# Optimization experiments

Measured on AMD Instinct MI355X. Metric: run time of the kernel, lower is better.

Reference implementation:

```python
import jax, jax.numpy as jnp
import numpy as np

G, N, F_IN, H, C = 128, 512, 128, 128, 10
LAMB = 1.0
NEG_SLOPE = 0.2
P_EDGE = 32.0 / N  # avg degree ~32


def setup_inputs() -> dict:
    key = jax.random.key(0)
    ks = jax.random.split(key, 12)
    x = jax.random.normal(ks[0], (G, N, F_IN), dtype=jnp.float32)
    # symmetric 0/1 adjacency without self loops (per-graph dense block)
    a = (jax.random.uniform(ks[1], (G, N, N)) < P_EDGE).astype(jnp.float32)
    adj = jnp.maximum(a, jnp.swapaxes(a, 1, 2)) * (1.0 - jnp.eye(N, dtype=jnp.float32))

    def lin(k, fi, fo):
        return (jax.random.normal(k, (fi, fo), dtype=jnp.float32) / np.float32(np.sqrt(fi)))

    return {
        "x": x, "adj": adj,
        "W1": lin(ks[2], F_IN, H), "b1": jnp.zeros((H,), jnp.float32),
        "W2": lin(ks[3], H, H), "b2": jnp.zeros((H,), jnp.float32),
        "W3": lin(ks[4], H, H), "b3": jnp.zeros((H,), jnp.float32),
        "att1_s": 0.1 * jax.random.normal(ks[5], (H,), dtype=jnp.float32),
        "att1_d": 0.1 * jax.random.normal(ks[6], (H,), dtype=jnp.float32),
        "att2_s": 0.1 * jax.random.normal(ks[7], (H,), dtype=jnp.float32),
        "att2_d": 0.1 * jax.random.normal(ks[8], (H,), dtype=jnp.float32),
        "Wl1": lin(ks[9], 2 * H, H), "bl1": jnp.zeros((H,), jnp.float32),
        "Wl2": lin(ks[10], H, H // 2), "bl2": jnp.zeros((H // 2,), jnp.float32),
        "Wl3": lin(ks[11], H // 2, C), "bl3": jnp.zeros((C,), jnp.float32),
    }


def gcn(x, adj, W, b):
    # GCNConv: D^{-1/2} (A + I) D^{-1/2} X W + b  (self-loop weight 1, edge weights in adj)
    deg = adj.sum(-1) + 1.0                              # [G, n]
    dinv = jax.lax.rsqrt(deg)
    xw = x @ W                                           # [G, n, H]
    agg = jnp.einsum('gij,gjf->gif', adj, dinv[..., None] * xw)
    return dinv[..., None] * agg + (dinv * dinv)[..., None] * xw + b


def info_score(x, adj):
    # HGP-SL node information score: row-wise L1 norm of (I - D^{-1} A) X
    deg = jnp.maximum(adj.sum(-1), 1.0)
    agg = jnp.einsum('gij,gjf->gif', adj, x) / deg[..., None]
    return jnp.sum(jnp.abs(x - agg), axis=-1)            # [G, n]


def hgpsl_pool(x, adj, att_s, att_d, k):
    # top-k node selection by information score, then structure learning:
    # dense (sample=False) path: e_ij = leaky_relu(att.[x_i||x_j]) + lamb*A_ij, softmax over j
    s = info_score(x, adj)
    _, idx = jax.lax.top_k(s, k)                         # [G, k]
    xk = jnp.take_along_axis(x, idx[..., None], axis=1)  # [G, k, H]
    g = jnp.arange(x.shape[0])[:, None, None]
    ak = adj[g, idx[:, :, None], idx[:, None, :]]        # induced adjacency [G, k, k]
    e = jax.nn.leaky_relu((xk @ att_s)[:, :, None] + (xk @ att_d)[:, None, :], NEG_SLOPE)
    attn = jax.nn.softmax(e + LAMB * ak, axis=-1)        # new learned edge weights
    return xk, attn


def readout(x):
    # gmp || gap over nodes
    return jnp.concatenate([x.max(axis=1), x.mean(axis=1)], axis=-1)


def reference(x, adj, W1, b1, W2, b2, W3, b3, att1_s, att1_d, att2_s, att2_d,
              Wl1, bl1, Wl2, bl2, Wl3, bl3):
    h = jax.nn.relu(gcn(x, adj, W1, b1))
    h, a1 = hgpsl_pool(h, adj, att1_s, att1_d, N // 2)
    x1 = readout(h)
    h = jax.nn.relu(gcn(h, a1, W2, b2))
    h, a2 = hgpsl_pool(h, a1, att2_s, att2_d, N // 4)
    x2 = readout(h)
    h = jax.nn.relu(gcn(h, a2, W3, b3))
    x3 = readout(h)
    z = jax.nn.relu(x1) + jax.nn.relu(x2) + jax.nn.relu(x3)
    z = jax.nn.relu(z @ Wl1 + bl1)
    z = jax.nn.relu(z @ Wl2 + bl2)
    return jax.nn.softmax(z @ Wl3 + bl3, axis=-1)
```

## Files before the change

kernel.cpp:

```cpp
#include <hip/hip_runtime.h>

#define Gg   128
#define N1   512
#define FH   128
#define K1   256
#define K2   128

typedef __bf16 bf16x8 __attribute__((ext_vector_type(8)));
typedef float  floatx4 __attribute__((ext_vector_type(4)));

__device__ inline float wredsum(float v) {
#pragma unroll
    for (int o = 32; o; o >>= 1) v += __shfl_xor(v, o, 64);
    return v;
}
__device__ inline float wredmax(float v) {
#pragma unroll
    for (int o = 32; o; o >>= 1) v = fmaxf(v, __shfl_xor(v, o, 64));
    return v;
}
__device__ inline unsigned short bf_rne(float x) {
    unsigned u = __float_as_uint(x);
    return (unsigned short)((u + 0x7fffu + ((u >> 16) & 1u)) >> 16);
}

__global__ __launch_bounds__(256) void k_prep(const float* __restrict__ adj,
        float* __restrict__ dinv_gcn, float* __restrict__ dinv_info) {
    int wave = threadIdx.x >> 6, lane = threadIdx.x & 63;
    long long row = (long long)blockIdx.x * 4 + wave;
    const float* ar = adj + row * N1;
    float s = 0.f;
#pragma unroll
    for (int c = 0; c < 2; ++c) {
        float4 v = *(const float4*)(ar + lane * 8 + c * 4);
        s += (v.x + v.y) + (v.z + v.w);
    }
    s = wredsum(s);
    if (lane == 0) {
        dinv_gcn[row]  = rsqrtf(s + 1.0f);
        dinv_info[row] = 1.0f / fmaxf(s, 1.0f);
    }
}

__global__ __launch_bounds__(256) void k_tsplit(const float* __restrict__ feat,
        unsigned short* __restrict__ Thi, unsigned short* __restrict__ Tmid,
        unsigned short* __restrict__ Tlo) {
    __shared__ float tile[64 * 65];
    int b = blockIdx.x;
    int g = b >> 4, rb = (b >> 1) & 7, cb = b & 1;
    int t = threadIdx.x;
    {
        int r0 = t >> 4, c4 = t & 15;
#pragma unroll
        for (int i = 0; i < 4; ++i) {
            int r = r0 + i * 16;
            float4 v = *(const float4*)(feat + ((long long)g * 512 + rb * 64 + r) * 128 + cb * 64 + c4 * 4);
            tile[r * 65 + c4 * 4 + 0] = v.x;
            tile[r * 65 + c4 * 4 + 1] = v.y;
            tile[r * 65 + c4 * 4 + 2] = v.z;
            tile[r * 65 + c4 * 4 + 3] = v.w;
        }
    }
    __syncthreads();
    int tf = t >> 2, chunk = t & 3;
    unsigned short hbuf[16] __attribute__((aligned(16)));
    unsigned short mbuf[16] __attribute__((aligned(16)));
    unsigned short lbuf[16] __attribute__((aligned(16)));
#pragma unroll
    for (int i = 0; i < 16; ++i) {
        int m = chunk * 16 + i;
        float v = tile[m * 65 + tf];
        unsigned short h = bf_rne(v);
        float fh = __uint_as_float((unsigned)h << 16);
        float r1 = v - fh;
        unsigned short md = bf_rne(r1);
        float fm = __uint_as_float((unsigned)md << 16);
        float r2 = r1 - fm;
        unsigned short lo = bf_rne(r2);
        hbuf[i] = h; mbuf[i] = md; lbuf[i] = lo;
    }
    long long obase = ((long long)g * 128 + cb * 64 + tf) * 512 + rb * 64 + chunk * 16;
    *(uint4*)(Thi + obase)      = *(const uint4*)&hbuf[0];
    *(uint4*)(Thi + obase + 8)  = *(const uint4*)&hbuf[8];
    *(uint4*)(Tmid + obase)     = *(const uint4*)&mbuf[0];
    *(uint4*)(Tmid + obase + 8) = *(const uint4*)&mbuf[8];
    *(uint4*)(Tlo + obase)      = *(const uint4*)&lbuf[0];
    *(uint4*)(Tlo + obase + 8)  = *(const uint4*)&lbuf[8];
}

template<int EPI>
__global__ __launch_bounds__(256) void k_aggmm(const float* __restrict__ adjf,
        const unsigned short* __restrict__ Bhi, const unsigned short* __restrict__ Bmid,
        const unsigned short* __restrict__ Blo,
        const float* __restrict__ dvec, const float* __restrict__ hx,
        const float* __restrict__ bias, float* __restrict__ outH, float* __restrict__ outS) {
    __shared__ unsigned short Al[128 * 40];
    __shared__ unsigned short Bls[3][128 * 40];
    __shared__ float sred[2][128];
    int b = blockIdx.x;
    int g  = (b & 7) + ((b >> 5) << 3);
    int rb = (b >> 3) & 3;
    int tid = threadIdx.x;
    int w = tid >> 6, lane = tid & 63;
    int wm = w >> 1, wn = w & 1;
    int ln = lane & 15, quad = lane >> 4;
    floatx4 acc[4][4];
#pragma unroll
    for (int i = 0; i < 4; ++i)
#pragma unroll
        for (int j = 0; j < 4; ++j) { floatx4 z = {0.f, 0.f, 0.f, 0.f}; acc[i][j] = z; }

    const long long arow0 = ((long long)g * 512 + rb * 128) * 512;
    for (int kk = 0; kk < 512; kk += 32) {
        __syncthreads();
#pragma unroll
        for (int i = 0; i < 4; ++i) {
            int id = tid + i * 256;
            int r = id >> 3, c = id & 7;
            float4 v = *(const float4*)(adjf + arow0 + (long long)r * 512 + kk + c * 4);
            ushort4 u;
            u.x = (unsigned short)(__float_as_uint(v.x) >> 16);
            u.y = (unsigned short)(__float_as_uint(v.y) >> 16);
            u.z = (unsigned short)(__float_as_uint(v.z) >> 16);
            u.w = (unsigned short)(__float_as_uint(v.w) >> 16);
            *(ushort4*)&Al[r * 40 + c * 4] = u;
        }
#pragma unroll
        for (int mB = 0; mB < 3; ++mB) {
            const unsigned short* Bp = (mB == 0) ? Bhi : (mB == 1 ? Bmid : Blo);
#pragma unroll
            for (int i = 0; i < 2; ++i) {
                int id = tid + i * 256;
                int r = id >> 2, c = id & 3;
                uint4 u = *(const uint4*)(Bp + ((long long)g * 128 + r) * 512 + kk + c * 8);
                *(uint4*)&Bls[mB][r * 40 + c * 8] = u;
            }
        }
        __syncthreads();
        bf16x8 af[4];
#pragma unroll
        for (int tm = 0; tm < 4; ++tm)
            af[tm] = *(const bf16x8*)&Al[(wm * 64 + tm * 16 + ln) * 40 + quad * 8];
#pragma unroll
        for (int s = 0; s < 3; ++s) {
#pragma unroll
            for (int tn = 0; tn < 4; ++tn) {
                bf16x8 bfr = *(const bf16x8*)&Bls[s][(wn * 64 + tn * 16 + ln) * 40 + quad * 8];
#pragma unroll
                for (int tm = 0; tm < 4; ++tm)
                    acc[tm][tn] = __builtin_amdgcn_mfma_f32_16x16x32_bf16(af[tm], bfr, acc[tm][tn], 0, 0, 0);
            }
        }
    }
    long long rowbase = (long long)g * 512 + rb * 128;
    if (EPI == 0) {
#pragma unroll
        for (int tm = 0; tm < 4; ++tm)
#pragma unroll
        for (int r = 0; r < 4; ++r) {
            int ml = wm * 64 + tm * 16 + quad * 4 + r;
            long long grow = rowbase + ml;
            float di = dvec[grow];
#pragma unroll
            for (int tn = 0; tn < 4; ++tn) {
                int nc = wn * 64 + tn * 16 + ln;
                float hv = hx[grow * 128 + nc];
                float o = fmaxf(fmaf(di, acc[tm][tn][r] + hv, bias[nc]), 0.f);
                outH[grow * 128 + nc] = o;
            }
        }
    } else {
#pragma unroll
        for (int tm = 0; tm < 4; ++tm)
#pragma unroll
        for (int r = 0; r < 4; ++r) {
            int ml = wm * 64 + tm * 16 + quad * 4 + r;
            long long grow = rowbase + ml;
            float di = dvec[grow];
            float v = 0.f;
#pragma unroll
            for (int tn = 0; tn < 4; ++tn) {
                int nc = wn * 64 + tn * 16 + ln;
                float hv = hx[grow * 128 + nc];
                v += fabsf(hv - acc[tm][tn][r] * di);
            }
            v += __shfl_xor(v, 1); v += __shfl_xor(v, 2);
            v += __shfl_xor(v, 4); v += __shfl_xor(v, 8);
            if (ln == 0) sred[wn][ml] = v;
        }
        __syncthreads();
        if (tid < 128) outS[rowbase + tid] = sred[0][tid] + sred[1][tid];
    }
}

__global__ __launch_bounds__(256) void k_gemm_rw(const float* __restrict__ A,
        const float* __restrict__ W, float* __restrict__ C,
        const float* __restrict__ rs) {
    __shared__ float Al[64][68];
    __shared__ float Wl[64][132];
    long long row0 = (long long)blockIdx.x * 64;
    int tid = threadIdx.x, tr = tid >> 4, tc = tid & 15;
    float acc[4][8] = {};
    for (int ch = 0; ch < 2; ++ch) {
        for (int p = tid; p < 1024; p += 256) {
            int r = p >> 4, c4 = p & 15;
            *(float4*)&Al[r][c4 * 4] = *(const float4*)(A + (row0 + r) * 128 + ch * 64 + c4 * 4);
        }
        for (int p = tid; p < 2048; p += 256) {
            int r = p >> 5, c4 = p & 31;
            *(float4*)&Wl[r][c4 * 4] = *(const float4*)(W + (ch * 64 + r) * 128 + c4 * 4);
        }
        __syncthreads();
        for (int k = 0; k < 64; ++k) {
            float4 w0 = *(const float4*)&Wl[k][tc * 8];
            float4 w1 = *(const float4*)&Wl[k][tc * 8 + 4];
            float w[8] = {w0.x, w0.y, w0.z, w0.w, w1.x, w1.y, w1.z, w1.w};
#pragma unroll
            for (int i = 0; i < 4; ++i) {
                float a = Al[tr * 4 + i][k];
#pragma unroll
                for (int j = 0; j < 8; ++j) acc[i][j] = fmaf(a, w[j], acc[i][j]);
            }
        }
        __syncthreads();
    }
#pragma unroll
    for (int i = 0; i < 4; ++i) {
        long long r = row0 + tr * 4 + i;
        float sc = rs ? rs[r] : 1.0f;
        *(float4*)(C + r * 128 + tc * 8)     = make_float4(sc * acc[i][0], sc * acc[i][1], sc * acc[i][2], sc * acc[i][3]);
        *(float4*)(C + r * 128 + tc * 8 + 4) = make_float4(sc * acc[i][4], sc * acc[i][5], sc * acc[i][6], sc * acc[i][7]);
    }
}

template<int NT, int KSEL>
__global__ __launch_bounds__(256) void k_topk(const float* __restrict__ s, int* __restrict__ idx) {
    __shared__ unsigned long long keys[NT];
    int g = blockIdx.x;
    const float* sg = s + g * NT;
    for (int t = threadIdx.x; t < NT; t += 256) {
        unsigned int b = __float_as_uint(sg[t]);
        unsigned int ord = (b & 0x80000000u) ? ~b : (b | 0x80000000u);
        keys[t] = ((unsigned long long)(~ord) << 32) | (unsigned int)t;
    }
    __syncthreads();
    for (int k = 2; k <= NT; k <<= 1) {
        for (int j = k >> 1; j > 0; j >>= 1) {
            for (int i = threadIdx.x; i < NT; i += 256) {
                int l = i ^ j;
                if (l > i) {
                    bool dir = ((i & k) == 0);
                    unsigned long long a = keys[i], b2 = keys[l];
                    bool sw = dir ? (a > b2) : (a < b2);
                    if (sw) { keys[i] = b2; keys[l] = a; }
                }
            }
            __syncthreads();
        }
    }
    for (int t = threadIdx.x; t < KSEL; t += 256)
        idx[g * KSEL + t] = (int)(keys[t] & 0xffffffffu);
}

template<int KK>
__global__ __launch_bounds__(256) void k_gather(const float* __restrict__ h, int srcN,
        const int* __restrict__ idx, const float* __restrict__ atts, const float* __restrict__ attd,
        float* __restrict__ xk, float* __restrict__ as_, float* __restrict__ ad_) {
    int wave = threadIdx.x >> 6, lane = threadIdx.x & 63;
    int r = blockIdx.x * 4 + wave;
    int g = r / KK;
    int j = idx[r];
    float2 v = *(const float2*)(h + ((long long)g * srcN + j) * 128 + lane * 2);
    *(float2*)(xk + (long long)r * 128 + lane * 2) = v;
    float2 sv = *(const float2*)(atts + lane * 2);
    float2 dv = *(const float2*)(attd + lane * 2);
    float ps = v.x * sv.x + v.y * sv.y;
    float pd = v.x * dv.x + v.y * dv.y;
    ps = wredsum(ps); pd = wredsum(pd);
    if (lane == 0) { as_[r] = ps; ad_[r] = pd; }
}

template<int KK, int SRCN>
__global__ __launch_bounds__(256) void k_attn(const float* __restrict__ adjSrc,
        const int* __restrict__ idx, const float* __restrict__ as_, const float* __restrict__ ad_,
        float* __restrict__ attn, float* __restrict__ dgo, float* __restrict__ dio) {
    constexpr int E = KK / 64;
    __shared__ int   idxL[KK];
    __shared__ float adL[KK];
    __shared__ float rowL[4][SRCN];
    int bpg = KK / 4;
    int g = blockIdx.x / bpg;
    int wave = threadIdx.x >> 6, lane = threadIdx.x & 63;
    int i = (blockIdx.x % bpg) * 4 + wave;
    for (int t = threadIdx.x; t < KK; t += 256) { idxL[t] = idx[g * KK + t]; adL[t] = ad_[g * KK + t]; }
    __syncthreads();
    int ri = idxL[i];
    const float* arow = adjSrc + ((long long)g * SRCN + ri) * SRCN;
    for (int c = lane; c < SRCN; c += 64) rowL[wave][c] = arow[c];
    float asi = as_[g * KK + i];
    float vals[E];
    float m = -1e30f;
#pragma unroll
    for (int e = 0; e < E; ++e) {
        int j = e * 64 + lane;
        float x = asi + adL[j];
        x = (x >= 0.f) ? x : 0.2f * x;
        x += rowL[wave][idxL[j]];
        vals[e] = x; m = fmaxf(m, x);
    }
    m = wredmax(m);
    float S = 0.f;
#pragma unroll
    for (int e = 0; e < E; ++e) { vals[e] = expf(vals[e] - m); S += vals[e]; }
    S = wredsum(S);
    float inv = 1.f / S, rs = 0.f;
    float* orow = attn + ((long long)g * KK + i) * KK;
#pragma unroll
    for (int e = 0; e < E; ++e) { float p = vals[e] * inv; rs += p; orow[e * 64 + lane] = p; }
    rs = wredsum(rs);
    if (lane == 0) { dgo[g * KK + i] = rsqrtf(rs + 1.f); dio[g * KK + i] = 1.f / fmaxf(rs, 1.f); }
}

template<int KK>
__global__ __launch_bounds__(128) void k_readout(const float* __restrict__ xk, float* __restrict__ xo) {
    int g = blockIdx.x, f = threadIdx.x;
    const float* p = xk + (long long)g * KK * 128 + f;
    float m = -1e30f, s = 0.f;
    for (int r = 0; r < KK; ++r) { float v = p[r * 128]; m = fmaxf(m, v); s += v; }
    xo[g * 256 + f] = m;
    xo[g * 256 + 128 + f] = s * (1.0f / KK);
}

template<int KK, bool SCALEY, int EPI>
__global__ __launch_bounds__(256) void k_agg(const float* __restrict__ A, const float* __restrict__ Y,
        const float* __restrict__ dg, const float* __restrict__ di_,
        const float* __restrict__ bias, const float* __restrict__ hx,
        float* __restrict__ outH, float* __restrict__ outS) {
    __shared__ float Al[64][68];
    __shared__ float Yl[64][132];
    __shared__ float red[64][17];
    constexpr int RB = KK / 64;
    int g = blockIdx.x / RB;
    int rb = blockIdx.x % RB;
    const float* Ag = A + (long long)g * KK * KK;
    const float* Yg = Y + (long long)g * KK * 128;
    int tid = threadIdx.x, tr = tid >> 4, tc = tid & 15;
    float acc[4][8] = {};
    for (int ch = 0; ch < KK / 64; ++ch) {
        for (int p = tid; p < 1024; p += 256) {
            int r = p >> 4, c4 = p & 15;
            *(float4*)&Al[r][c4 * 4] = *(const float4*)(Ag + (rb * 64 + r) * KK + ch * 64 + c4 * 4);
        }
        for (int p = tid; p < 2048; p += 256) {
            int r = p >> 5, c4 = p & 31;
            float4 v = *(const float4*)(Yg + (ch * 64 + r) * 128 + c4 * 4);
            if (SCALEY) { float sc = dg[g * KK + ch * 64 + r]; v.x *= sc; v.y *= sc; v.z *= sc; v.w *= sc; }
            *(float4*)&Yl[r][c4 * 4] = v;
        }
        __syncthreads();
        for (int k = 0; k < 64; ++k) {
            float4 w0 = *(const float4*)&Yl[k][tc * 8];
            float4 w1 = *(const float4*)&Yl[k][tc * 8 + 4];
            float w[8] = {w0.x, w0.y, w0.z, w0.w, w1.x, w1.y, w1.z, w1.w};
#pragma unroll
            for (int i = 0; i < 4; ++i) {
                float a = Al[tr * 4 + i][k];
#pragma unroll
                for (int j = 0; j < 8; ++j) acc[i][j] = fmaf(a, w[j], acc[i][j]);
            }
        }
        __syncthreads();
    }
    int i0 = rb * 64 + tr * 4;
    if (EPI == 0) {
#pragma unroll
        for (int i = 0; i < 4; ++i) {
            long long gi = (long long)g * KK + i0 + i;
            float d = dg[gi], dd = d * d;
            float4 x0 = *(const float4*)(hx + gi * 128 + tc * 8);
            float4 x1 = *(const float4*)(hx + gi * 128 + tc * 8 + 4);
            float4 b0 = *(const float4*)(bias + tc * 8);
            float4 b1 = *(const float4*)(bias + tc * 8 + 4);
            float4 o0, o1;
            o0.x = fmaxf(fmaf(d, acc[i][0], fmaf(dd, x0.x, b0.x)), 0.f);
            o0.y = fmaxf(fmaf(d, acc[i][1], fmaf(dd, x0.y, b0.y)), 0.f);
            o0.z = fmaxf(fmaf(d, acc[i][2], fmaf(dd, x0.z, b0.z)), 0.f);
            o0.w = fmaxf(fmaf(d, acc[i][3], fmaf(dd, x0.w, b0.w)), 0.f);
            o1.x = fmaxf(fmaf(d, acc[i][4], fmaf(dd, x1.x, b1.x)), 0.f);
            o1.y = fmaxf(fmaf(d, acc[i][5], fmaf(dd, x1.y, b1.y)), 0.f);
            o1.z = fmaxf(fmaf(d, acc[i][6], fmaf(dd, x1.z, b1.z)), 0.f);
            o1.w = fmaxf(fmaf(d, acc[i][7], fmaf(dd, x1.w, b1.w)), 0.f);
            *(float4*)(outH + gi * 128 + tc * 8)     = o0;
            *(float4*)(outH + gi * 128 + tc * 8 + 4) = o1;
        }
    } else {
#pragma unroll
        for (int i = 0; i < 4; ++i) {
            long long gi = (long long)g * KK + i0 + i;
            float d = di_[gi];
            float4 x0 = *(const float4*)(hx + gi * 128 + tc * 8);
            float4 x1 = *(const float4*)(hx + gi * 128 + tc * 8 + 4);
            float p = fabsf(x0.x - acc[i][0] * d) + fabsf(x0.y - acc[i][1] * d)
                    + fabsf(x0.z - acc[i][2] * d) + fabsf(x0.w - acc[i][3] * d)
                    + fabsf(x1.x - acc[i][4] * d) + fabsf(x1.y - acc[i][5] * d)
                    + fabsf(x1.z - acc[i][6] * d) + fabsf(x1.w - acc[i][7] * d);
            red[tr * 4 + i][tc] = p;
        }
        __syncthreads();
        if (tid < 64) {
            float s = 0.f;
#pragma unroll
            for (int t = 0; t < 16; ++t) s += red[tid][t];
            outS[(long long)g * KK + rb * 64 + tid] = s;
        }
    }
}

__global__ __launch_bounds__(128) void k_mlp(const float* __restrict__ x1, const float* __restrict__ x2,
        const float* __restrict__ x3,
        const float* __restrict__ Wl1, const float* __restrict__ bl1,
        const float* __restrict__ Wl2, const float* __restrict__ bl2,
        const float* __restrict__ Wl3, const float* __restrict__ bl3,
        float* __restrict__ out) {
    __shared__ float z[256], z1[128], z2[64], lg[10];
    int g = blockIdx.x, t = threadIdx.x;
    for (int k = t; k < 256; k += 128)
        z[k] = fmaxf(x1[g * 256 + k], 0.f) + fmaxf(x2[g * 256 + k], 0.f) + fmaxf(x3[g * 256 + k], 0.f);
    __syncthreads();
    {
        float acc = bl1[t];
        for (int k = 0; k < 256; ++k) acc = fmaf(z[k], Wl1[k * 128 + t], acc);
        z1[t] = fmaxf(acc, 0.f);
    }
    __syncthreads();
    if (t < 64) {
        float acc = bl2[t];
        for (int k = 0; k < 128; ++k) acc = fmaf(z1[k], Wl2[k * 64 + t], acc);
        z2[t] = fmaxf(acc, 0.f);
    }
    __syncthreads();
    if (t < 10) {
        float acc = bl3[t];
        for (int k = 0; k < 64; ++k) acc = fmaf(z2[k], Wl3[k * 10 + t], acc);
        lg[t] = acc;
    }
    __syncthreads();
    if (t == 0) {
        float m = -1e30f;
        for (int c = 0; c < 10; ++c) m = fmaxf(m, lg[c]);
        float S = 0.f;
        float e[10];
        for (int c = 0; c < 10; ++c) { e[c] = expf(lg[c] - m); S += e[c]; }
        float inv = 1.f / S;
        for (int c = 0; c < 10; ++c) out[g * 10 + c] = e[c] * inv;
    }
}

extern "C" void kernel_launch(void* const* d_in, const int* in_sizes, int n_in,
                              void* d_out, int out_size, void* d_ws, size_t ws_size,
                              hipStream_t stream) {
    const float* x     = (const float*)d_in[0];
    const float* adj   = (const float*)d_in[1];
    const float* W1    = (const float*)d_in[2];
    const float* b1    = (const float*)d_in[3];
    const float* W2    = (const float*)d_in[4];
    const float* b2    = (const float*)d_in[5];
    const float* W3    = (const float*)d_in[6];
    const float* b3    = (const float*)d_in[7];
    const float* att1s = (const float*)d_in[8];
    const float* att1d = (const float*)d_in[9];
    const float* att2s = (const float*)d_in[10];
    const float* att2d = (const float*)d_in[11];
    const float* Wl1   = (const float*)d_in[12];
    const float* bl1   = (const float*)d_in[13];
    const float* Wl2   = (const float*)d_in[14];
    const float* bl2   = (const float*)d_in[15];
    const float* Wl3   = (const float*)d_in[16];
    const float* bl3   = (const float*)d_in[17];
    float* out = (float*)d_out;

    char* ws = (char*)d_ws;
    unsigned short* Thi  = (unsigned short*)(ws + 0);
    unsigned short* Tmid = (unsigned short*)(ws + 16777216);
    unsigned short* Tlo  = (unsigned short*)(ws + 33554432);
    float* xk1 = (float*)(ws + 0);
    float* xw2 = (float*)(ws + 16777216);
    float* h2  = (float*)(ws + 33554432);
    float* xk2 = (float*)(ws + 16777216);
    float* a2  = (float*)(ws + 25165824);
    float* xw3 = (float*)(ws + 0);
    float* h3  = (float*)(ws + 8388608);
    float* dxw1 = (float*)(ws + 50331648);
    float* h1   = dxw1;
    float* a1   = dxw1;
    float* s1      = (float*)(ws + 83886080);
    int*   idx1    = (int*)  (ws + 84148224);
    float* as1     = (float*)(ws + 84279296);
    float* ad1     = (float*)(ws + 84410368);
    float* dinv_g1 = (float*)(ws + 84541440);
    float* dinv_i1 = (float*)(ws + 84803584);
    float* dinv_g2 = (float*)(ws + 85065728);
    float* dinv_i2 = (float*)(ws + 85196800);
    float* x1r     = (float*)(ws + 85327872);
    float* s2      = (float*)(ws + 85458944);
    int*   idx2    = (int*)  (ws + 85590016);
    float* as2     = (float*)(ws + 85655552);
    float* ad2     = (float*)(ws + 85721088);
    float* dinv_g3 = (float*)(ws + 85786624);
    float* dinv_i3 = (float*)(ws + 85852160);
    float* x2r     = (float*)(ws + 85917696);
    float* x3r     = (float*)(ws + 86048768);

    k_prep<<<Gg * N1 / 4, 256, 0, stream>>>(adj, dinv_g1, dinv_i1);
    k_gemm_rw<<<Gg * N1 / 64, 256, 0, stream>>>(x, W1, dxw1, dinv_g1);
    k_tsplit<<<Gg * 16, 256, 0, stream>>>(dxw1, Thi, Tmid, Tlo);
    k_aggmm<0><<<Gg * 4, 256, 0, stream>>>(adj, Thi, Tmid, Tlo, dinv_g1, dxw1, b1, h1, nullptr);
    k_tsplit<<<Gg * 16, 256, 0, stream>>>(h1, Thi, Tmid, Tlo);
    k_aggmm<1><<<Gg * 4, 256, 0, stream>>>(adj, Thi, Tmid, Tlo, dinv_i1, h1, nullptr, nullptr, s1);
    k_topk<N1, K1><<<Gg, 256, 0, stream>>>(s1, idx1);
    k_gather<K1><<<Gg * K1 / 4, 256, 0, stream>>>(h1, N1, idx1, att1s, att1d, xk1, as1, ad1);
    k_readout<K1><<<Gg, 128, 0, stream>>>(xk1, x1r);
    k_attn<K1, N1><<<Gg * K1 / 4, 256, 0, stream>>>(adj, idx1, as1, ad1, a1, dinv_g2, dinv_i2);

    k_gemm_rw<<<Gg * K1 / 64, 256, 0, stream>>>(xk1, W2, xw2, nullptr);
    k_agg<K1, true, 0><<<Gg * (K1 / 64), 256, 0, stream>>>(a1, xw2, dinv_g2, dinv_i2, b2, xw2, h2, nullptr);
    k_agg<K1, false, 1><<<Gg * (K1 / 64), 256, 0, stream>>>(a1, h2, dinv_g2, dinv_i2, b2, h2, nullptr, s2);
    k_topk<K1, K2><<<Gg, 256, 0, stream>>>(s2, idx2);
    k_gather<K2><<<Gg * K2 / 4, 256, 0, stream>>>(h2, K1, idx2, att2s, att2d, xk2, as2, ad2);
    k_readout<K2><<<Gg, 128, 0, stream>>>(xk2, x2r);
    k_attn<K2, K1><<<Gg * K2 / 4, 256, 0, stream>>>(a1, idx2, as2, ad2, a2, dinv_g3, dinv_i3);

    k_gemm_rw<<<Gg * K2 / 64, 256, 0, stream>>>(xk2, W3, xw3, nullptr);
    k_agg<K2, true, 0><<<Gg * (K2 / 64), 256, 0, stream>>>(a2, xw3, dinv_g3, dinv_i3, b3, xw3, h3, nullptr);
    k_readout<K2><<<Gg, 128, 0, stream>>>(h3, x3r);

    k_mlp<<<Gg, 128, 0, stream>>>(x1r, x2r, x3r, Wl1, bl1, Wl2, bl2, Wl3, bl3, out);
}
```

Before: 606.8 us.

## Compress adjacency to bitmasks and feed MFMA aggregation from bits

The prep kernel now also packs each adjacency row into a 512-bit mask via wave ballots. The two first-level aggregation GEMMs expand these bits into bf16 ones in registers and read the B operands directly from global memory instead of staging them through LDS. They use smaller 64-row tiles, giving twice as many blocks. The first attention kernel looks up edges in the bitmask instead of gathering from the dense fp32 adjacency, and the workspace is re-laid out so the split buffers are not aliased. This removes repeated reads of the 128MB fp32 adjacency, at the cost of uncached, non-LDS B loads that are re-read per block, and it assumes the adjacency holds only 0/1 values.

```diff
diff --git a/kernel.cpp b/kernel.cpp
--- a/kernel.cpp
+++ b/kernel.cpp
@@ -6,6 +6,7 @@
 #define K1   256
 #define K2   128
 
+typedef unsigned short ush;
 typedef __bf16 bf16x8 __attribute__((ext_vector_type(8)));
 typedef float  floatx4 __attribute__((ext_vector_type(4)));
 
@@ -19,177 +20,39 @@
     for (int o = 32; o; o >>= 1) v = fmaxf(v, __shfl_xor(v, o, 64));
     return v;
 }
-__device__ inline unsigned short bf_rne(float x) {
+__device__ inline ush bf_rne(float x) {
     unsigned u = __float_as_uint(x);
-    return (unsigned short)((u + 0x7fffu + ((u >> 16) & 1u)) >> 16);
+    return (ush)((u + 0x7fffu + ((u >> 16) & 1u)) >> 16);
+}
+__device__ inline float bf2f(ush u) { return __uint_as_float((unsigned)u << 16); }
+__device__ inline void split3(float v, ush& h, ush& m, ush& l) {
+    h = bf_rne(v);
+    float r1 = v - bf2f(h);
+    m = bf_rne(r1);
+    l = bf_rne(r1 - bf2f(m));
 }
 
 __global__ __launch_bounds__(256) void k_prep(const float* __restrict__ adj,
-        float* __restrict__ dinv_gcn, float* __restrict__ dinv_info) {
+        float* __restrict__ dinv_gcn, float* __restrict__ dinv_info,
+        unsigned* __restrict__ adjbits) {
     int wave = threadIdx.x >> 6, lane = threadIdx.x & 63;
     long long row = (long long)blockIdx.x * 4 + wave;
     const float* ar = adj + row * N1;
     float s = 0.f;
-#pragma unroll
-    for (int c = 0; c < 2; ++c) {
-        float4 v = *(const float4*)(ar + lane * 8 + c * 4);
-        s += (v.x + v.y) + (v.z + v.w);
-    }
+    unsigned myw = 0;
+#pragma unroll
+    for (int c = 0; c < 8; ++c) {
+        float v = ar[c * 64 + lane];
+        s += v;
+        unsigned long long mk = __ballot(v != 0.0f);
+        unsigned lo = (unsigned)mk, hi = (unsigned)(mk >> 32);
+        if ((lane >> 1) == c) myw = (lane & 1) ? hi : lo;
+    }
+    if (lane < 16) adjbits[row * 16 + lane] = myw;
     s = wredsum(s);
     if (lane == 0) {
         dinv_gcn[row]  = rsqrtf(s + 1.0f);
         dinv_info[row] = 1.0f / fmaxf(s, 1.0f);
-    }
-}
-
-__global__ __launch_bounds__(256) void k_tsplit(const float* __restrict__ feat,
-        unsigned short* __restrict__ Thi, unsigned short* __restrict__ Tmid,
-        unsigned short* __restrict__ Tlo) {
-    __shared__ float tile[64 * 65];
-    int b = blockIdx.x;
-    int g = b >> 4, rb = (b >> 1) & 7, cb = b & 1;
-    int t = threadIdx.x;
-    {
-        int r0 = t >> 4, c4 = t & 15;
-#pragma unroll
-        for (int i = 0; i < 4; ++i) {
-            int r = r0 + i * 16;
-            float4 v = *(const float4*)(feat + ((long long)g * 512 + rb * 64 + r) * 128 + cb * 64 + c4 * 4);
-            tile[r * 65 + c4 * 4 + 0] = v.x;
-            tile[r * 65 + c4 * 4 + 1] = v.y;
-            tile[r * 65 + c4 * 4 + 2] = v.z;
-            tile[r * 65 + c4 * 4 + 3] = v.w;
-        }
-    }
-    __syncthreads();
-    int tf = t >> 2, chunk = t & 3;
-    unsigned short hbuf[16] __attribute__((aligned(16)));
-    unsigned short mbuf[16] __attribute__((aligned(16)));
-    unsigned short lbuf[16] __attribute__((aligned(16)));
-#pragma unroll
-    for (int i = 0; i < 16; ++i) {
-        int m = chunk * 16 + i;
-        float v = tile[m * 65 + tf];
-        unsigned short h = bf_rne(v);
-        float fh = __uint_as_float((unsigned)h << 16);
-        float r1 = v - fh;
-        unsigned short md = bf_rne(r1);
-        float fm = __uint_as_float((unsigned)md << 16);
-        float r2 = r1 - fm;
-        unsigned short lo = bf_rne(r2);
-        hbuf[i] = h; mbuf[i] = md; lbuf[i] = lo;
-    }
-    long long obase = ((long long)g * 128 + cb * 64 + tf) * 512 + rb * 64 + chunk * 16;
-    *(uint4*)(Thi + obase)      = *(const uint4*)&hbuf[0];
-    *(uint4*)(Thi + obase + 8)  = *(const uint4*)&hbuf[8];
-    *(uint4*)(Tmid + obase)     = *(const uint4*)&mbuf[0];
-    *(uint4*)(Tmid + obase + 8) = *(const uint4*)&mbuf[8];
-    *(uint4*)(Tlo + obase)      = *(const uint4*)&lbuf[0];
-    *(uint4*)(Tlo + obase + 8)  = *(const uint4*)&lbuf[8];
-}
-
-template<int EPI>
-__global__ __launch_bounds__(256) void k_aggmm(const float* __restrict__ adjf,
-        const unsigned short* __restrict__ Bhi, const unsigned short* __restrict__ Bmid,
-        const unsigned short* __restrict__ Blo,
-        const float* __restrict__ dvec, const float* __restrict__ hx,
-        const float* __restrict__ bias, float* __restrict__ outH, float* __restrict__ outS) {
-    __shared__ unsigned short Al[128 * 40];
-    __shared__ unsigned short Bls[3][128 * 40];
-    __shared__ float sred[2][128];
-    int b = blockIdx.x;
-    int g  = (b & 7) + ((b >> 5) << 3);
-    int rb = (b >> 3) & 3;
-    int tid = threadIdx.x;
-    int w = tid >> 6, lane = tid & 63;
-    int wm = w >> 1, wn = w & 1;
-    int ln = lane & 15, quad = lane >> 4;
-    floatx4 acc[4][4];
-#pragma unroll
-    for (int i = 0; i < 4; ++i)
-#pragma unroll
-        for (int j = 0; j < 4; ++j) { floatx4 z = {0.f, 0.f, 0.f, 0.f}; acc[i][j] = z; }
-
-    const long long arow0 = ((long long)g * 512 + rb * 128) * 512;
-    for (int kk = 0; kk < 512; kk += 32) {
-        __syncthreads();
-#pragma unroll
-        for (int i = 0; i < 4; ++i) {
-            int id = tid + i * 256;
-            int r = id >> 3, c = id & 7;
-            float4 v = *(const float4*)(adjf + arow0 + (long long)r * 512 + kk + c * 4);
-            ushort4 u;
-            u.x = (unsigned short)(__float_as_uint(v.x) >> 16);
-            u.y = (unsigned short)(__float_as_uint(v.y) >> 16);
-            u.z = (unsigned short)(__float_as_uint(v.z) >> 16);
-            u.w = (unsigned short)(__float_as_uint(v.w) >> 16);
-            *(ushort4*)&Al[r * 40 + c * 4] = u;
-        }
-#pragma unroll
-        for (int mB = 0; mB < 3; ++mB) {
-            const unsigned short* Bp = (mB == 0) ? Bhi : (mB == 1 ? Bmid : Blo);
-#pragma unroll
-            for (int i = 0; i < 2; ++i) {
-                int id = tid + i * 256;
-                int r = id >> 2, c = id & 3;
-                uint4 u = *(const uint4*)(Bp + ((long long)g * 128 + r) * 512 + kk + c * 8);
-                *(uint4*)&Bls[mB][r * 40 + c * 8] = u;
-            }
-        }
-        __syncthreads();
-        bf16x8 af[4];
-#pragma unroll
-        for (int tm = 0; tm < 4; ++tm)
-            af[tm] = *(const bf16x8*)&Al[(wm * 64 + tm * 16 + ln) * 40 + quad * 8];
-#pragma unroll
-        for (int s = 0; s < 3; ++s) {
-#pragma unroll
-            for (int tn = 0; tn < 4; ++tn) {
-                bf16x8 bfr = *(const bf16x8*)&Bls[s][(wn * 64 + tn * 16 + ln) * 40 + quad * 8];
-#pragma unroll
-                for (int tm = 0; tm < 4; ++tm)
-                    acc[tm][tn] = __builtin_amdgcn_mfma_f32_16x16x32_bf16(af[tm], bfr, acc[tm][tn], 0, 0, 0);
-            }
-        }
-    }
-    long long rowbase = (long long)g * 512 + rb * 128;
-    if (EPI == 0) {
-#pragma unroll
-        for (int tm = 0; tm < 4; ++tm)
-#pragma unroll
-        for (int r = 0; r < 4; ++r) {
-            int ml = wm * 64 + tm * 16 + quad * 4 + r;
-            long long grow = rowbase + ml;
-            float di = dvec[grow];
-#pragma unroll
-            for (int tn = 0; tn < 4; ++tn) {
-                int nc = wn * 64 + tn * 16 + ln;
-                float hv = hx[grow * 128 + nc];
-                float o = fmaxf(fmaf(di, acc[tm][tn][r] + hv, bias[nc]), 0.f);
-                outH[grow * 128 + nc] = o;
-            }
-        }
-    } else {
-#pragma unroll
-        for (int tm = 0; tm < 4; ++tm)
-#pragma unroll
-        for (int r = 0; r < 4; ++r) {
-            int ml = wm * 64 + tm * 16 + quad * 4 + r;
-            long long grow = rowbase + ml;
-            float di = dvec[grow];
-            float v = 0.f;
-#pragma unroll
-            for (int tn = 0; tn < 4; ++tn) {
-                int nc = wn * 64 + tn * 16 + ln;
-                float hv = hx[grow * 128 + nc];
-                v += fabsf(hv - acc[tm][tn][r] * di);
-            }
-            v += __shfl_xor(v, 1); v += __shfl_xor(v, 2);
-            v += __shfl_xor(v, 4); v += __shfl_xor(v, 8);
-            if (ln == 0) sred[wn][ml] = v;
-        }
-        __syncthreads();
-        if (tid < 128) outS[rowbase + tid] = sred[0][tid] + sred[1][tid];
     }
 }
 
@@ -230,6 +93,137 @@
         float sc = rs ? rs[r] : 1.0f;
         *(float4*)(C + r * 128 + tc * 8)     = make_float4(sc * acc[i][0], sc * acc[i][1], sc * acc[i][2], sc * acc[i][3]);
         *(float4*)(C + r * 128 + tc * 8 + 4) = make_float4(sc * acc[i][4], sc * acc[i][5], sc * acc[i][6], sc * acc[i][7]);
+    }
+}
+
+__global__ __launch_bounds__(256) void k_tsplit(const float* __restrict__ feat,
+        ush* __restrict__ Thi, ush* __restrict__ Tmid, ush* __restrict__ Tlo) {
+    __shared__ float tile[64 * 65];
+    int b = blockIdx.x;
+    int g = b >> 4, rb = (b >> 1) & 7, cb = b & 1;
+    int t = threadIdx.x;
+    {
+        int r0 = t >> 4, c4 = t & 15;
+#pragma unroll
+        for (int i = 0; i < 4; ++i) {
+            int r = r0 + i * 16;
+            float4 v = *(const float4*)(feat + ((long long)g * 512 + rb * 64 + r) * 128 + cb * 64 + c4 * 4);
+            tile[r * 65 + c4 * 4 + 0] = v.x;
+            tile[r * 65 + c4 * 4 + 1] = v.y;
+            tile[r * 65 + c4 * 4 + 2] = v.z;
+            tile[r * 65 + c4 * 4 + 3] = v.w;
+        }
+    }
+    __syncthreads();
+    int tf = t >> 2, chunk = t & 3;
+    ush hbuf[16] __attribute__((aligned(16)));
+    ush mbuf[16] __attribute__((aligned(16)));
+    ush lbuf[16] __attribute__((aligned(16)));
+#pragma unroll
+    for (int i = 0; i < 16; ++i) {
+        int m = chunk * 16 + i;
+        split3(tile[m * 65 + tf], hbuf[i], mbuf[i], lbuf[i]);
+    }
+    long long obase = ((long long)g * 128 + cb * 64 + tf) * 512 + rb * 64 + chunk * 16;
+    *(uint4*)(Thi + obase)      = *(const uint4*)&hbuf[0];
+    *(uint4*)(Thi + obase + 8)  = *(const uint4*)&hbuf[8];
+    *(uint4*)(Tmid + obase)     = *(const uint4*)&mbuf[0];
+    *(uint4*)(Tmid + obase + 8) = *(const uint4*)&mbuf[8];
+    *(uint4*)(Tlo + obase)      = *(const uint4*)&lbuf[0];
+    *(uint4*)(Tlo + obase + 8)  = *(const uint4*)&lbuf[8];
+}
+
+template<int EPI>
+__global__ __launch_bounds__(256) void k_aggb(const unsigned* __restrict__ adjbits,
+        const ush* __restrict__ Bhi, const ush* __restrict__ Bmid, const ush* __restrict__ Blo,
+        const float* __restrict__ dvec, const float* __restrict__ hx,
+        const float* __restrict__ bias, float* __restrict__ outH, float* __restrict__ outS) {
+    __shared__ unsigned bitsL[64 * 17];
+    __shared__ float sred[2][64];
+    int b = blockIdx.x;
+    int g  = (b & 7) + ((b >> 6) << 3);
+    int rb = (b >> 3) & 7;
+    int tid = threadIdx.x;
+    int w = tid >> 6, lane = tid & 63;
+    int wm = w >> 1, wn = w & 1;
+    int ln = lane & 15, quad = lane >> 4;
+    {
+        int r = tid >> 2, w4 = (tid & 3) * 4;
+        uint4 v = *(const uint4*)(adjbits + ((long long)(g * 512 + rb * 64 + r)) * 16 + w4);
+        bitsL[r * 17 + w4 + 0] = v.x; bitsL[r * 17 + w4 + 1] = v.y;
+        bitsL[r * 17 + w4 + 2] = v.z; bitsL[r * 17 + w4 + 3] = v.w;
+    }
+    __syncthreads();
+    floatx4 acc[2][4];
+#pragma unroll
+    for (int i = 0; i < 2; ++i)
+#pragma unroll
+        for (int j = 0; j < 4; ++j) { floatx4 z = {0.f, 0.f, 0.f, 0.f}; acc[i][j] = z; }
+
+    const long long bb = (long long)g * 128 * 512;
+    for (int kt = 0; kt < 16; ++kt) {
+        int kk = kt * 32;
+        bf16x8 af[2];
+#pragma unroll
+        for (int tm = 0; tm < 2; ++tm) {
+            unsigned word = bitsL[(wm * 32 + tm * 16 + ln) * 17 + kt];
+            unsigned byte = (word >> (quad * 8)) & 0xffu;
+            unsigned au[4] __attribute__((aligned(16)));
+            au[0] = ((byte >> 0) & 1 ? 0x3F80u : 0u) | ((byte >> 1) & 1 ? 0x3F800000u : 0u);
+            au[1] = ((byte >> 2) & 1 ? 0x3F80u : 0u) | ((byte >> 3) & 1 ? 0x3F800000u : 0u);
+            au[2] = ((byte >> 4) & 1 ? 0x3F80u : 0u) | ((byte >> 5) & 1 ? 0x3F800000u : 0u);
+            au[3] = ((byte >> 6) & 1 ? 0x3F80u : 0u) | ((byte >> 7) & 1 ? 0x3F800000u : 0u);
+            af[tm] = *(const bf16x8*)au;
+        }
+#pragma unroll
+        for (int tn = 0; tn < 4; ++tn) {
+            long long off = bb + (long long)(wn * 64 + tn * 16 + ln) * 512 + kk + quad * 8;
+            bf16x8 bh = *(const bf16x8*)(Bhi + off);
+            bf16x8 bm = *(const bf16x8*)(Bmid + off);
+            bf16x8 bl = *(const bf16x8*)(Blo + off);
+#pragma unroll
+            for (int tm = 0; tm < 2; ++tm) {
+                acc[tm][tn] = __builtin_amdgcn_mfma_f32_16x16x32_bf16(af[tm], bh, acc[tm][tn], 0, 0, 0);
+                acc[tm][tn] = __builtin_amdgcn_mfma_f32_16x16x32_bf16(af[tm], bm, acc[tm][tn], 0, 0, 0);
+                acc[tm][tn] = __builtin_amdgcn_mfma_f32_16x16x32_bf16(af[tm], bl, acc[tm][tn], 0, 0, 0);
+            }
+        }
+    }
+    long long rowbase = (long long)g * 512 + rb * 64;
+    if (EPI == 0) {
+#pragma unroll
+        for (int tm = 0; tm < 2; ++tm)
+#pragma unroll
+        for (int r = 0; r < 4; ++r) {
+            long long grow = rowbase + wm * 32 + tm * 16 + quad * 4 + r;
+            float di = dvec[grow];
+#pragma unroll
+            for (int tn = 0; tn < 4; ++tn) {
+                int nc = wn * 64 + tn * 16 + ln;
+                outH[grow * 128 + nc] =
+                    fmaxf(fmaf(di, acc[tm][tn][r] + hx[grow * 128 + nc], bias[nc]), 0.f);
+            }
+        }
+    } else {
+#pragma unroll
+        for (int tm = 0; tm < 2; ++tm)
+#pragma unroll
+        for (int r = 0; r < 4; ++r) {
+            int ml = wm * 32 + tm * 16 + quad * 4 + r;
+            long long grow = rowbase + ml;
+            float di = dvec[grow];
+            float v = 0.f;
+#pragma unroll
+            for (int tn = 0; tn < 4; ++tn) {
+                int nc = wn * 64 + tn * 16 + ln;
+                v += fabsf(hx[grow * 128 + nc] - acc[tm][tn][r] * di);
+            }
+            v += __shfl_xor(v, 1); v += __shfl_xor(v, 2);
+            v += __shfl_xor(v, 4); v += __shfl_xor(v, 8);
+            if (ln == 0) sred[wn][ml] = v;
+        }
+        __syncthreads();
+        if (tid < 64) outS[rowbase + tid] = sred[0][tid] + sred[1][tid];
     }
 }
 
@@ -278,6 +272,50 @@
     float pd = v.x * dv.x + v.y * dv.y;
     ps = wredsum(ps); pd = wredsum(pd);
     if (lane == 0) { as_[r] = ps; ad_[r] = pd; }
+}
+
+__global__ __launch_bounds__(256) void k_attn1b(const unsigned* __restrict__ adjbits,
+        const int* __restrict__ idx, const float* __restrict__ as_, const float* __restrict__ ad_,
+        float* __restrict__ a1, float* __restrict__ dgo, float* __restrict__ dio) {
+    __shared__ int   idxL[K1];
+    __shared__ float adL[K1];
+    __shared__ unsigned bitsW[4][20];
+    int g = blockIdx.x / (K1 / 4);
+    int wave = threadIdx.x >> 6, lane = threadIdx.x & 63;
+    int i = (blockIdx.x % (K1 / 4)) * 4 + wave;
+    for (int t = threadIdx.x; t < K1; t += 256) { idxL[t] = idx[g * K1 + t]; adL[t] = ad_[g * K1 + t]; }
+    __syncthreads();
+    int ri = idxL[i];
+    if (lane < 4) {
+        uint4 v = *(const uint4*)(adjbits + ((long long)(g * 512 + ri)) * 16 + lane * 4);
+        bitsW[wave][lane * 4 + 0] = v.x; bitsW[wave][lane * 4 + 1] = v.y;
+        bitsW[wave][lane * 4 + 2] = v.z; bitsW[wave][lane * 4 + 3] = v.w;
+    }
+    __syncthreads();
+    float asi = as_[g * K1 + i];
+    float vals[4];
+    float m = -1e30f;
+#pragma unroll
+    for (int e = 0; e < 4; ++e) {
+        int j = e * 64 + lane;
+        float x = asi + adL[j];
+        x = (x >= 0.f) ? x : 0.2f * x;
+        int jj = idxL[j];
+        unsigned bit = (bitsW[wave][jj >> 5] >> (jj & 31)) & 1u;
+        x += (float)bit;
+        vals[e] = x; m = fmaxf(m, x);
+    }
+    m = wredmax(m);
+    float S = 0.f;
+#pragma unroll
+    for (int e = 0; e < 4; ++e) { vals[e] = expf(vals[e] - m); S += vals[e]; }
+    S = wredsum(S);
+    float inv = 1.f / S, rs = 0.f;
+    float* orow = a1 + ((long long)g * K1 + i) * K1;
+#pragma unroll
+    for (int e = 0; e < 4; ++e) { float p = vals[e] * inv; rs += p; orow[e * 64 + lane] = p; }
+    rs = wredsum(rs);
+    if (lane == 0) { dgo[g * K1 + i] = rsqrtf(rs + 1.f); dio[g * K1 + i] = 1.f / fmaxf(rs, 1.f); }
 }
 
 template<int KK, int SRCN>
@@ -480,47 +518,51 @@
     float* out = (float*)d_out;
 
     char* ws = (char*)d_ws;
-    unsigned short* Thi  = (unsigned short*)(ws + 0);
-    unsigned short* Tmid = (unsigned short*)(ws + 16777216);
-    unsigned short* Tlo  = (unsigned short*)(ws + 33554432);
-    float* xk1 = (float*)(ws + 0);
-    float* xw2 = (float*)(ws + 16777216);
-    float* h2  = (float*)(ws + 33554432);
-    float* xk2 = (float*)(ws + 16777216);
-    float* a2  = (float*)(ws + 25165824);
-    float* xw3 = (float*)(ws + 0);
-    float* h3  = (float*)(ws + 8388608);
-    float* dxw1 = (float*)(ws + 50331648);
-    float* h1   = dxw1;
-    float* a1   = dxw1;
-    float* s1      = (float*)(ws + 83886080);
-    int*   idx1    = (int*)  (ws + 84148224);
-    float* as1     = (float*)(ws + 84279296);
-    float* ad1     = (float*)(ws + 84410368);
-    float* dinv_g1 = (float*)(ws + 84541440);
-    float* dinv_i1 = (float*)(ws + 84803584);
-    float* dinv_g2 = (float*)(ws + 85065728);
-    float* dinv_i2 = (float*)(ws + 85196800);
-    float* x1r     = (float*)(ws + 85327872);
-    float* s2      = (float*)(ws + 85458944);
-    int*   idx2    = (int*)  (ws + 85590016);
-    float* as2     = (float*)(ws + 85655552);
-    float* ad2     = (float*)(ws + 85721088);
-    float* dinv_g3 = (float*)(ws + 85786624);
-    float* dinv_i3 = (float*)(ws + 85852160);
-    float* x2r     = (float*)(ws + 85917696);
-    float* x3r     = (float*)(ws + 86048768);
-
-    k_prep<<<Gg * N1 / 4, 256, 0, stream>>>(adj, dinv_g1, dinv_i1);
+    unsigned* adjbits = (unsigned*)(ws + 0);
+    ush*   T1hi   = (ush*)  (ws + 8388608);
+    ush*   T1mid  = (ush*)  (ws + 25165824);
+    ush*   T1lo   = (ush*)  (ws + 41943040);
+    ush*   T2hi   = (ush*)  (ws + 58720256);
+    ush*   T2mid  = (ush*)  (ws + 75497472);
+    ush*   T2lo   = (ush*)  (ws + 92274688);
+    float* dxw1   = (float*)(ws + 109051904);
+    float* h1     = dxw1;
+    float* a1     = (float*)(ws + 142606336);
+    float* xk1    = (float*)(ws + 176160768);
+    float* xw2    = (float*)(ws + 192937984);
+    float* h2     = (float*)(ws + 209715200);
+    float* xk2    = (float*)(ws + 226492416);
+    float* a2     = (float*)(ws + 234881024);
+    float* xw3    = (float*)(ws + 243269632);
+    float* h3     = (float*)(ws + 251658240);
+    float* s1     = (float*)(ws + 260046848);
+    int*   idx1   = (int*)  (ws + 260308992);
+    float* as1    = (float*)(ws + 260571136);
+    float* ad1    = (float*)(ws + 260702208);
+    float* dinv_g1= (float*)(ws + 260833280);
+    float* dinv_i1= (float*)(ws + 261095424);
+    float* dinv_g2= (float*)(ws + 261357568);
+    float* dinv_i2= (float*)(ws + 261488640);
+    float* x1r    = (float*)(ws + 261619712);
+    float* s2     = (float*)(ws + 261750784);
+    int*   idx2   = (int*)  (ws + 261881856);
+    float* as2    = (float*)(ws + 261947392);
+    float* ad2    = (float*)(ws + 262012928);
+    float* dinv_g3= (float*)(ws + 262078464);
+    float* dinv_i3= (float*)(ws + 262144000);
+    float* x2r    = (float*)(ws + 262209536);
+    float* x3r    = (float*)(ws + 262340608);
+
+    k_prep<<<Gg * N1 / 4, 256, 0, stream>>>(adj, dinv_g1, dinv_i1, adjbits);
     k_gemm_rw<<<Gg * N1 / 64, 256, 0, stream>>>(x, W1, dxw1, dinv_g1);
-    k_tsplit<<<Gg * 16, 256, 0, stream>>>(dxw1, Thi, Tmid, Tlo);
-    k_aggmm<0><<<Gg * 4, 256, 0, stream>>>(adj, Thi, Tmid, Tlo, dinv_g1, dxw1, b1, h1, nullptr);
-    k_tsplit<<<Gg * 16, 256, 0, stream>>>(h1, Thi, Tmid, Tlo);
-    k_aggmm<1><<<Gg * 4, 256, 0, stream>>>(adj, Thi, Tmid, Tlo, dinv_i1, h1, nullptr, nullptr, s1);
+    k_tsplit<<<Gg * 16, 256, 0, stream>>>(dxw1, T1hi, T1mid, T1lo);
+    k_aggb<0><<<Gg * 8, 256, 0, stream>>>(adjbits, T1hi, T1mid, T1lo, dinv_g1, dxw1, b1, h1, nullptr);
+    k_tsplit<<<Gg * 16, 256, 0, stream>>>(h1, T2hi, T2mid, T2lo);
+    k_aggb<1><<<Gg * 8, 256, 0, stream>>>(adjbits, T2hi, T2mid, T2lo, dinv_i1, h1, nullptr, nullptr, s1);
     k_topk<N1, K1><<<Gg, 256, 0, stream>>>(s1, idx1);
     k_gather<K1><<<Gg * K1 / 4, 256, 0, stream>>>(h1, N1, idx1, att1s, att1d, xk1, as1, ad1);
     k_readout<K1><<<Gg, 128, 0, stream>>>(xk1, x1r);
-    k_attn<K1, N1><<<Gg * K1 / 4, 256, 0, stream>>>(adj, idx1, as1, ad1, a1, dinv_g2, dinv_i2);
+    k_attn1b<<<Gg * K1 / 4, 256, 0, stream>>>(adjbits, idx1, as1, ad1, a1, dinv_g2, dinv_i2);
 
     k_gemm_rw<<<Gg * K1 / 64, 256, 0, stream>>>(xk1, W2, xw2, nullptr);
     k_agg<K1, true, 0><<<Gg * (K1 / 64), 256, 0, stream>>>(a1, xw2, dinv_g2, dinv_i2, b2, xw2, h2, nullptr);
```

After: 708.1 us. 16.7% more time.
